# Optimization experiments

Hardware: AMD Instinct MI355X
Metric: run time of the kernel (lower is better)

Reference implementation:

```python
import jax, jax.numpy as jnp
import numpy as np

B, C, H, W = 4, 256, 64, 64
NH, NQ, HD, WS = 4, 16, 64, 3   # num_heads, num_queries, head_dim, attn_window_size
PD = NH * HD                    # proj_dim = 256


def setup_inputs() -> dict:
    key = jax.random.key(0)
    ks = jax.random.split(key, 6)
    s = 0.02
    return {
        "x": jax.random.normal(ks[0], (B, C, H, W), jnp.float32),
        "kv_w": jax.random.normal(ks[1], (2 * PD, C), jnp.float32) * s,
        "dot_w": jax.random.normal(ks[2], (NH, NQ, HD), jnp.float32) * s,
        "head_w": jax.random.normal(ks[3], (HD, PD), jnp.float32) * s,
        "head_b": jnp.zeros((HD,), jnp.float32),
        "q_w": jax.random.normal(ks[4], (C, NQ * HD), jnp.float32) * s,
        "q_b": jnp.zeros((C,), jnp.float32),
    }


def _unfold(x, ws):
    """Sliding ws x ws patches over last two dims (stride 1, same padding).
    x: (..., h, w) -> (..., h, w, ws*ws), flattened in (i*ws + j) order
    matching torch's unfold(2).unfold(3)."""
    pad = ws // 2
    padw = [(0, 0)] * (x.ndim - 2) + [(pad, pad), (pad, pad)]
    xp = jnp.pad(x, padw)
    h, w = x.shape[-2], x.shape[-1]
    return jnp.stack(
        [xp[..., i:i + h, j:j + w] for i in range(ws) for j in range(ws)],
        axis=-1,
    )


def reference(x, kv_w, dot_w, head_w, head_b, q_w, q_b):
    b, c, h, w = x.shape
    # kv 1x1 conv, then split into k, v (each proj_dim channels)
    kv = jnp.einsum('oc,bchw->bohw', kv_w, x)
    k, v = jnp.split(kv, 2, axis=1)
    # grouped 1x1 conv: per-head head_dim -> num_queries (NOTE: no scale; the
    # original defines self.scale but never applies it in forward)
    kh = k.reshape(b, NH, HD, h, w)
    attn = jnp.einsum('bndhw,nqd->bnqhw', kh, dot_w)
    # unfold overlapping 3x3 windows (L = ws^2 = 9)
    attn_p = _unfold(attn, WS)                        # (b, n, q, h, w, L)
    v_p = _unfold(v.reshape(b, NH, HD, h, w), WS)     # (b, n, d, h, w, L)
    attn_p = jax.nn.softmax(attn_p, axis=-1)
    # per-pixel weighted sum over the window, arranged as (b, q, n, d, h, w)
    out = jnp.einsum('bnqhwl,bndhwl->bqndhw', attn_p, v_p)
    out = out.reshape(b, NQ, PD, h, w)                # (n d) -> proj_dim channels
    # head_proj: 1x1 conv proj_dim -> head_dim (dropout=0)
    y = jnp.einsum('op,bqphw->bqohw', head_w, out) + head_b[None, None, :, None, None]
    # query_proj: 1x1 conv (k*head_dim) -> dim (dropout=0)
    y = y.reshape(b, NQ * HD, h, w)
    z = jnp.einsum('oc,bchw->bohw', q_w, y) + q_b[None, :, None, None]
    return z
```

## Files before the change

### kernel.cpp

```cpp
#include <hip/hip_runtime.h>
#include <hip/hip_bf16.h>
#include <cstdint>

typedef __hip_bfloat16 bf16;
using bf16x8 = __attribute__((ext_vector_type(8))) short;
using f32x4  = __attribute__((ext_vector_type(4))) float;

#define HW_T 4096
#define B_T  4

__device__ __forceinline__ short f2bs(float f) {
    bf16 h = __float2bfloat16(f);
    return *reinterpret_cast<short*>(&h);
}
__device__ __forceinline__ float bs2f(short s) {
    unsigned int u = ((unsigned int)(unsigned short)s) << 16;
    float f;
    __builtin_memcpy(&f, &u, 4);
    return f;
}

__global__ __launch_bounds__(256) void fuse_all(
    const float* __restrict__ kv_w, const float* __restrict__ dot_w,
    const float* __restrict__ head_w, const float* __restrict__ q_w,
    bf16* __restrict__ Wf, bf16* __restrict__ qwF)
{
    const int rb = blockIdx.x;
    if (rb < 320) {
        const int r = rb, c = threadIdx.x;
        float acc = 0.f;
        if (r < 64) {
            const int n = r >> 4, q = r & 15;
            #pragma unroll 8
            for (int d = 0; d < 64; ++d)
                acc += dot_w[(n * 16 + q) * 64 + d] * kv_w[(size_t)(n * 64 + d) * 256 + c];
        } else {
            const int rr = r - 64, n = rr >> 6, dh = rr & 63;
            #pragma unroll 8
            for (int dd = 0; dd < 64; ++dd)
                acc += head_w[dh * 256 + n * 64 + dd] * kv_w[(size_t)(256 + n * 64 + dd) * 256 + c];
        }
        Wf[((size_t)(c >> 3) * 320 + r) * 8 + (c & 7)] = __float2bfloat16(acc);
    } else {
        const int t  = (rb - 320) * 256 + threadIdx.x;
        const int ch = t & 255, kb = t >> 8;
        const float* src = q_w + (size_t)ch * 1024 + kb * 8;
        bf16x8 pk;
        #pragma unroll
        for (int j = 0; j < 8; ++j) pk[j] = f2bs(src[j]);
        *(bf16x8*)&qwF[(size_t)t * 8] = pk;
    }
}

__global__ __launch_bounds__(256) void gemm_xw(
    const float* __restrict__ x, const bf16* __restrict__ Wf,
    bf16* __restrict__ AH)
{
    __shared__ __align__(16) bf16 As[2][4][32][8];
    const int tid  = threadIdx.x;
    const int lane = tid & 63;
    const int wave = tid >> 6;
    const int p0 = blockIdx.x * 32;
    const int b  = blockIdx.y;
    const float* xb = x + (size_t)b * 256 * HW_T;
    const int fi = lane & 15, quad = lane >> 4;
    const int wn0 = wave * 80;

    const int spx = tid & 31, sk = (tid >> 5) * 4;

    f32x4 acc[2][5] = {};
    float xr[4];
    bf16x8 bcur[5], bnxt[5];

    {
        const float* xp = xb + (size_t)sk * HW_T + p0 + spx;
        #pragma unroll
        for (int j = 0; j < 4; ++j) xr[j] = xp[(size_t)j * HW_T];
        #pragma unroll
        for (int j = 0; j < 5; ++j)
            bcur[j] = *(const bf16x8*)&Wf[((size_t)quad * 320 + wn0 + j * 16 + fi) * 8];
        short4 pk;
        pk.x = f2bs(xr[0]); pk.y = f2bs(xr[1]); pk.z = f2bs(xr[2]); pk.w = f2bs(xr[3]);
        *(short4*)&As[0][sk >> 3][spx][sk & 7] = pk;
    }

    for (int it = 0; it < 8; ++it) {
        const int cur = it & 1;
        __syncthreads();
        if (it < 7) {
            const int k1 = (it + 1) * 32;
            const float* xp = xb + (size_t)(k1 + sk) * HW_T + p0 + spx;
            #pragma unroll
            for (int j = 0; j < 4; ++j) xr[j] = xp[(size_t)j * HW_T];
            const size_t kb = (size_t)(k1 >> 3) + quad;
            #pragma unroll
            for (int j = 0; j < 5; ++j)
                bnxt[j] = *(const bf16x8*)&Wf[(kb * 320 + wn0 + j * 16 + fi) * 8];
        }
        bf16x8 af[2];
        #pragma unroll
        for (int i = 0; i < 2; ++i)
            af[i] = *(const bf16x8*)&As[cur][quad][i * 16 + fi][0];
        #pragma unroll
        for (int i = 0; i < 2; ++i)
            #pragma unroll
            for (int j = 0; j < 5; ++j)
                acc[i][j] = __builtin_amdgcn_mfma_f32_16x16x32_bf16(
                    af[i], bcur[j], acc[i][j], 0, 0, 0);
        if (it < 7) {
            short4 pk;
            pk.x = f2bs(xr[0]); pk.y = f2bs(xr[1]); pk.z = f2bs(xr[2]); pk.w = f2bs(xr[3]);
            *(short4*)&As[cur ^ 1][sk >> 3][spx][sk & 7] = pk;
            #pragma unroll
            for (int j = 0; j < 5; ++j) bcur[j] = bnxt[j];
        }
    }

    bf16* Cp = AH + ((size_t)b * HW_T + p0) * 320;
    #pragma unroll
    for (int i = 0; i < 2; ++i) {
        const int pl = i * 16 + quad * 4;
        #pragma unroll
        for (int r = 0; r < 4; ++r)
            #pragma unroll
            for (int j = 0; j < 5; ++j)
                Cp[(size_t)(pl + r) * 320 + wn0 + j * 16 + fi] =
                    __float2bfloat16(acc[i][j][r]);
    }
}

#define YPAD 1032
#define ATTN_LDS (32 * YPAD * 2 + 4 * 9 * 64 * 4)

__global__ __launch_bounds__(256) void attn_qy(
    const bf16* __restrict__ AH, const float* __restrict__ head_b,
    const bf16* __restrict__ qwF, const float* __restrict__ q_b,
    float* __restrict__ z)
{
    extern __shared__ __align__(16) char smem[];
    bf16*  yL = (bf16*)smem;
    float* Pm = (float*)(smem + 32 * YPAD * 2) + (threadIdx.x >> 6) * 9 * 64;

    const int tid  = threadIdx.x;
    const int wave = tid >> 6, lane = tid & 63;
    const int half = blockIdx.x & 1;
    const int h    = (blockIdx.x >> 1) & 63;
    const int b    = blockIdx.x >> 7;
    const int w0   = half * 32;
    const int hw0  = h * 64 + w0;
    const int fi = lane & 15, quad = lane >> 4;
    const ushort* AHu = (const ushort*)AH;

    float hb[4];
    #pragma unroll
    for (int dt = 0; dt < 4; ++dt) hb[dt] = head_b[dt * 16 + fi];

    for (int pi = 0; pi < 8; ++pi) {
        const int lp = wave * 8 + pi;
        const int w  = w0 + lp;
        int off[9]; float okf[9];
        #pragma unroll
        for (int l = 0; l < 9; ++l) {
            const int i = l / 3, j = l % 3;
            const int hh = h + i - 1, ww = w + j - 1;
            const bool ok = ((unsigned)hh < 64u) && ((unsigned)ww < 64u);
            off[l] = ((b << 12) + (ok ? hh : h) * 64 + (ok ? ww : w)) * 320;
            okf[l] = ok ? 1.0f : 0.0f;
        }
        {
            float lg[9];
            #pragma unroll
            for (int l = 0; l < 9; ++l)
                lg[l] = bs2f((short)AHu[(size_t)off[l] + lane]) * okf[l];
            float m = lg[0];
            #pragma unroll
            for (int l = 1; l < 9; ++l) m = fmaxf(m, lg[l]);
            float e[9], s = 0.f;
            #pragma unroll
            for (int l = 0; l < 9; ++l) { e[l] = __expf(lg[l] - m); s += e[l]; }
            const float inv = 1.0f / s;
            #pragma unroll
            for (int l = 0; l < 9; ++l) Pm[l * 64 + lane] = e[l] * inv * okf[l];
        }

        bf16x8 afr;
        #pragma unroll
        for (int j = 0; j < 8; ++j) {
            const int k = quad * 8 + j;
            afr[j] = f2bs(Pm[(k >> 2) * 64 + (k & 3) * 16 + fi]);
        }
        f32x4 acc[4];
        #pragma unroll
        for (int dt = 0; dt < 4; ++dt) {
            acc[dt][0] = hb[dt]; acc[dt][1] = hb[dt];
            acc[dt][2] = hb[dt]; acc[dt][3] = hb[dt];
        }
        #pragma unroll
        for (int dt = 0; dt < 4; ++dt) {
            bf16x8 bfr;
            #pragma unroll
            for (int j = 0; j < 8; ++j) {
                const int k = quad * 8 + j;
                bfr[j] = (short)AHu[(size_t)off[k >> 2] + 64 + (k & 3) * 64 + dt * 16 + fi];
            }
            acc[dt] = __builtin_amdgcn_mfma_f32_16x16x32_bf16(afr, bfr, acc[dt], 0, 0, 0);
        }
        #pragma unroll
        for (int n = 0; n < 4; ++n) {
            float pv[4];
            #pragma unroll
            for (int r = 0; r < 4; ++r) pv[r] = Pm[8 * 64 + n * 16 + quad * 4 + r];
            #pragma unroll
            for (int dt = 0; dt < 4; ++dt) {
                const float hval =
                    bs2f((short)AHu[(size_t)off[8] + 64 + n * 64 + dt * 16 + fi]);
                #pragma unroll
                for (int r = 0; r < 4; ++r) acc[dt][r] = fmaf(pv[r], hval, acc[dt][r]);
            }
        }
        #pragma unroll
        for (int dt = 0; dt < 4; ++dt)
            #pragma unroll
            for (int r = 0; r < 4; ++r)
                yL[(size_t)lp * YPAD + (quad * 4 + r) * 64 + dt * 16 + fi] =
                    __float2bfloat16(acc[dt][r]);
    }
    __syncthreads();

    f32x4 zacc[4][2] = {};
    bf16x8 af[4], afn[4];
    #pragma unroll
    for (int i = 0; i < 4; ++i)
        af[i] = *(const bf16x8*)&qwF[((size_t)quad * 256 + wave * 64 + i * 16 + fi) * 8];

    #pragma unroll 2
    for (int k0 = 0; k0 < 1024; k0 += 32) {
        if (k0 < 992) {
            const size_t kb = (size_t)((k0 + 32) >> 3) + quad;
            #pragma unroll
            for (int i = 0; i < 4; ++i)
                afn[i] = *(const bf16x8*)&qwF[(kb * 256 + wave * 64 + i * 16 + fi) * 8];
        }
        bf16x8 bfr[2];
        #pragma unroll
        for (int j = 0; j < 2; ++j)
            bfr[j] = *(const bf16x8*)&yL[(size_t)(j * 16 + fi) * YPAD + k0 + quad * 8];
        #pragma unroll
        for (int i = 0; i < 4; ++i)
            #pragma unroll
            for (int j = 0; j < 2; ++j)
                zacc[i][j] = __builtin_amdgcn_mfma_f32_16x16x32_bf16(
                    af[i], bfr[j], zacc[i][j], 0, 0, 0);
        #pragma unroll
        for (int i = 0; i < 4; ++i) af[i] = afn[i];
    }

    #pragma unroll
    for (int i = 0; i < 4; ++i) {
        const int row0 = wave * 64 + i * 16 + quad * 4;
        #pragma unroll
        for (int r = 0; r < 4; ++r) {
            const float bv = q_b[row0 + r];
            #pragma unroll
            for (int j = 0; j < 2; ++j)
                z[((size_t)(b * 256 + row0 + r)) * HW_T + hw0 + j * 16 + fi] =
                    zacc[i][j][r] + bv;
        }
    }
}

extern "C" void kernel_launch(void* const* d_in, const int* in_sizes, int n_in,
                              void* d_out, int out_size, void* d_ws, size_t ws_size,
                              hipStream_t stream) {
    (void)in_sizes; (void)n_in; (void)out_size; (void)ws_size;
    const float* x      = (const float*)d_in[0];
    const float* kv_w   = (const float*)d_in[1];
    const float* dot_w  = (const float*)d_in[2];
    const float* head_w = (const float*)d_in[3];
    const float* head_b = (const float*)d_in[4];
    const float* q_w    = (const float*)d_in[5];
    const float* q_b    = (const float*)d_in[6];
    float* z = (float*)d_out;

    char* ws   = (char*)d_ws;
    bf16*  AH  = (bf16*)ws;
    bf16*  qwF = (bf16*)(ws + 10485760);
    bf16*  Wf  = (bf16*)(ws + 11010048);

    static bool attr_done = []() {
        hipFuncSetAttribute((const void*)attn_qy,
                            hipFuncAttributeMaxDynamicSharedMemorySize, ATTN_LDS);
        return true;
    }();
    (void)attr_done;

    fuse_all<<<dim3(448), 256, 0, stream>>>(kv_w, dot_w, head_w, q_w, Wf, qwF);

    gemm_xw<<<dim3(128, B_T), 256, 0, stream>>>(x, Wf, AH);

    attn_qy<<<dim3(512), 256, ATTN_LDS, stream>>>(AH, head_b, qwF, q_b, z);
}
```

Before: 113.0 us.

## Interleave head-proj weights by head for vector loads; deepen GEMM K step to 64

Reorders the fused head-projection rows in Wf so each output dim's four per-head values sit next to each other. The attention kernel can then gather the MFMA B fragments and the ninth-tap values with ushort4 vector loads instead of scalar 16-bit loads. The x·W GEMM now processes 64 channels per iteration with 8-element bf16 LDS stores, halving loop trips and barriers. The cost is more registers for the doubled prefetch buffers, which could reduce occupancy.

```diff
diff --git a/kernel.cpp b/kernel.cpp
--- a/kernel.cpp
+++ b/kernel.cpp
@@ -13,8 +13,8 @@
     bf16 h = __float2bfloat16(f);
     return *reinterpret_cast<short*>(&h);
 }
-__device__ __forceinline__ float bs2f(short s) {
-    unsigned int u = ((unsigned int)(unsigned short)s) << 16;
+__device__ __forceinline__ float bs2f(unsigned short s) {
+    unsigned int u = ((unsigned int)s) << 16;
     float f;
     __builtin_memcpy(&f, &u, 4);
     return f;
@@ -29,18 +29,21 @@
     if (rb < 320) {
         const int r = rb, c = threadIdx.x;
         float acc = 0.f;
+        int rowIdx;
         if (r < 64) {
             const int n = r >> 4, q = r & 15;
             #pragma unroll 8
             for (int d = 0; d < 64; ++d)
                 acc += dot_w[(n * 16 + q) * 64 + d] * kv_w[(size_t)(n * 64 + d) * 256 + c];
+            rowIdx = r;
         } else {
             const int rr = r - 64, n = rr >> 6, dh = rr & 63;
             #pragma unroll 8
             for (int dd = 0; dd < 64; ++dd)
                 acc += head_w[dh * 256 + n * 64 + dd] * kv_w[(size_t)(256 + n * 64 + dd) * 256 + c];
-        }
-        Wf[((size_t)(c >> 3) * 320 + r) * 8 + (c & 7)] = __float2bfloat16(acc);
+            rowIdx = 64 + dh * 4 + n;
+        }
+        Wf[((size_t)(c >> 3) * 320 + rowIdx) * 8 + (c & 7)] = __float2bfloat16(acc);
     } else {
         const int t  = (rb - 320) * 256 + threadIdx.x;
         const int ch = t & 255, kb = t >> 8;
@@ -56,7 +59,7 @@
     const float* __restrict__ x, const bf16* __restrict__ Wf,
     bf16* __restrict__ AH)
 {
-    __shared__ __align__(16) bf16 As[2][4][32][8];
+    __shared__ __align__(16) bf16 As[2][8][32][8];
     const int tid  = threadIdx.x;
     const int lane = tid & 63;
     const int wave = tid >> 6;
@@ -66,53 +69,66 @@
     const int fi = lane & 15, quad = lane >> 4;
     const int wn0 = wave * 80;
 
-    const int spx = tid & 31, sk = (tid >> 5) * 4;
+    const int spx = tid & 31, sc8 = tid >> 5;
 
     f32x4 acc[2][5] = {};
-    float xr[4];
-    bf16x8 bcur[5], bnxt[5];
+    float xr[8];
+    bf16x8 bcur[2][5], bnxt[2][5];
 
     {
-        const float* xp = xb + (size_t)sk * HW_T + p0 + spx;
-        #pragma unroll
-        for (int j = 0; j < 4; ++j) xr[j] = xp[(size_t)j * HW_T];
-        #pragma unroll
-        for (int j = 0; j < 5; ++j)
-            bcur[j] = *(const bf16x8*)&Wf[((size_t)quad * 320 + wn0 + j * 16 + fi) * 8];
-        short4 pk;
-        pk.x = f2bs(xr[0]); pk.y = f2bs(xr[1]); pk.z = f2bs(xr[2]); pk.w = f2bs(xr[3]);
-        *(short4*)&As[0][sk >> 3][spx][sk & 7] = pk;
-    }
-
-    for (int it = 0; it < 8; ++it) {
+        const float* xp = xb + (size_t)(sc8 * 8) * HW_T + p0 + spx;
+        #pragma unroll
+        for (int j = 0; j < 8; ++j) xr[j] = xp[(size_t)j * HW_T];
+        #pragma unroll
+        for (int c = 0; c < 2; ++c)
+            #pragma unroll
+            for (int j = 0; j < 5; ++j)
+                bcur[c][j] = *(const bf16x8*)
+                    &Wf[((size_t)(c * 4 + quad) * 320 + wn0 + j * 16 + fi) * 8];
+        bf16x8 pk;
+        #pragma unroll
+        for (int j = 0; j < 8; ++j) pk[j] = f2bs(xr[j]);
+        *(bf16x8*)&As[0][sc8][spx][0] = pk;
+    }
+
+    #pragma unroll
+    for (int it = 0; it < 4; ++it) {
         const int cur = it & 1;
         __syncthreads();
-        if (it < 7) {
-            const int k1 = (it + 1) * 32;
-            const float* xp = xb + (size_t)(k1 + sk) * HW_T + p0 + spx;
-            #pragma unroll
-            for (int j = 0; j < 4; ++j) xr[j] = xp[(size_t)j * HW_T];
-            const size_t kb = (size_t)(k1 >> 3) + quad;
-            #pragma unroll
-            for (int j = 0; j < 5; ++j)
-                bnxt[j] = *(const bf16x8*)&Wf[(kb * 320 + wn0 + j * 16 + fi) * 8];
-        }
-        bf16x8 af[2];
-        #pragma unroll
-        for (int i = 0; i < 2; ++i)
-            af[i] = *(const bf16x8*)&As[cur][quad][i * 16 + fi][0];
-        #pragma unroll
-        for (int i = 0; i < 2; ++i)
-            #pragma unroll
-            for (int j = 0; j < 5; ++j)
-                acc[i][j] = __builtin_amdgcn_mfma_f32_16x16x32_bf16(
-                    af[i], bcur[j], acc[i][j], 0, 0, 0);
-        if (it < 7) {
-            short4 pk;
-            pk.x = f2bs(xr[0]); pk.y = f2bs(xr[1]); pk.z = f2bs(xr[2]); pk.w = f2bs(xr[3]);
-            *(short4*)&As[cur ^ 1][sk >> 3][spx][sk & 7] = pk;
-            #pragma unroll
-            for (int j = 0; j < 5; ++j) bcur[j] = bnxt[j];
+        if (it < 3) {
+            const int k1 = (it + 1) * 64;
+            const float* xp = xb + (size_t)(k1 + sc8 * 8) * HW_T + p0 + spx;
+            #pragma unroll
+            for (int j = 0; j < 8; ++j) xr[j] = xp[(size_t)j * HW_T];
+            #pragma unroll
+            for (int c = 0; c < 2; ++c)
+                #pragma unroll
+                for (int j = 0; j < 5; ++j)
+                    bnxt[c][j] = *(const bf16x8*)
+                        &Wf[((size_t)((k1 >> 3) + c * 4 + quad) * 320 + wn0 + j * 16 + fi) * 8];
+        }
+        #pragma unroll
+        for (int c = 0; c < 2; ++c) {
+            bf16x8 af[2];
+            #pragma unroll
+            for (int i = 0; i < 2; ++i)
+                af[i] = *(const bf16x8*)&As[cur][c * 4 + quad][i * 16 + fi][0];
+            #pragma unroll
+            for (int i = 0; i < 2; ++i)
+                #pragma unroll
+                for (int j = 0; j < 5; ++j)
+                    acc[i][j] = __builtin_amdgcn_mfma_f32_16x16x32_bf16(
+                        af[i], bcur[c][j], acc[i][j], 0, 0, 0);
+        }
+        if (it < 3) {
+            bf16x8 pk;
+            #pragma unroll
+            for (int j = 0; j < 8; ++j) pk[j] = f2bs(xr[j]);
+            *(bf16x8*)&As[cur ^ 1][sc8][spx][0] = pk;
+            #pragma unroll
+            for (int c = 0; c < 2; ++c)
+                #pragma unroll
+                for (int j = 0; j < 5; ++j) bcur[c][j] = bnxt[c][j];
         }
     }
 
@@ -171,7 +187,7 @@
             float lg[9];
             #pragma unroll
             for (int l = 0; l < 9; ++l)
-                lg[l] = bs2f((short)AHu[(size_t)off[l] + lane]) * okf[l];
+                lg[l] = bs2f(AHu[(size_t)off[l] + lane]) * okf[l];
             float m = lg[0];
             #pragma unroll
             for (int l = 1; l < 9; ++l) m = fmaxf(m, lg[l]);
@@ -197,25 +213,37 @@
         }
         #pragma unroll
         for (int dt = 0; dt < 4; ++dt) {
+            const int d = dt * 16 + fi;
+            const ushort4 u0 = *(const ushort4*)&AHu[(size_t)off[quad * 2]     + 64 + d * 4];
+            const ushort4 u1 = *(const ushort4*)&AHu[(size_t)off[quad * 2 + 1] + 64 + d * 4];
             bf16x8 bfr;
-            #pragma unroll
-            for (int j = 0; j < 8; ++j) {
-                const int k = quad * 8 + j;
-                bfr[j] = (short)AHu[(size_t)off[k >> 2] + 64 + (k & 3) * 64 + dt * 16 + fi];
-            }
+            bfr[0] = (short)u0.x; bfr[1] = (short)u0.y;
+            bfr[2] = (short)u0.z; bfr[3] = (short)u0.w;
+            bfr[4] = (short)u1.x; bfr[5] = (short)u1.y;
+            bfr[6] = (short)u1.z; bfr[7] = (short)u1.w;
             acc[dt] = __builtin_amdgcn_mfma_f32_16x16x32_bf16(afr, bfr, acc[dt], 0, 0, 0);
         }
-        #pragma unroll
-        for (int n = 0; n < 4; ++n) {
-            float pv[4];
-            #pragma unroll
-            for (int r = 0; r < 4; ++r) pv[r] = Pm[8 * 64 + n * 16 + quad * 4 + r];
+        {
+            float pv[4][4];
+            #pragma unroll
+            for (int n = 0; n < 4; ++n)
+                #pragma unroll
+                for (int r = 0; r < 4; ++r)
+                    pv[n][r] = Pm[8 * 64 + n * 16 + quad * 4 + r];
             #pragma unroll
             for (int dt = 0; dt < 4; ++dt) {
-                const float hval =
-                    bs2f((short)AHu[(size_t)off[8] + 64 + n * 64 + dt * 16 + fi]);
-                #pragma unroll
-                for (int r = 0; r < 4; ++r) acc[dt][r] = fmaf(pv[r], hval, acc[dt][r]);
+                const int d = dt * 16 + fi;
+                const ushort4 u = *(const ushort4*)&AHu[(size_t)off[8] + 64 + d * 4];
+                const float h0 = bs2f(u.x), h1 = bs2f(u.y), h2 = bs2f(u.z), h3 = bs2f(u.w);
+                #pragma unroll
+                for (int r = 0; r < 4; ++r) {
+                    float a = acc[dt][r];
+                    a = fmaf(pv[0][r], h0, a);
+                    a = fmaf(pv[1][r], h1, a);
+                    a = fmaf(pv[2][r], h2, a);
+                    a = fmaf(pv[3][r], h3, a);
+                    acc[dt][r] = a;
+                }
             }
         }
         #pragma unroll
```

New measurement: 112.7 us. About the same (-0.2%).
